# Kernel optimization log

Measured on AMD Instinct MI355X. Metric: run time of the kernel, lower is better.

The kernel has to match this reference:

```python
import jax, jax.numpy as jnp
import numpy as np

HIDDEN = 1024
VOCAB = 50257
MAX_LEN = 12


def setup_inputs() -> dict:
    key = jax.random.key(0)
    ks = jax.random.split(key, 16)
    H, V, L = HIDDEN, VOCAB, MAX_LEN
    s = 1.0 / np.sqrt(H)
    inp = {
        "input": jax.random.randint(ks[0], (1, 1), 0, V, dtype=jnp.int64),
        "h_hidden": jax.random.normal(ks[1], (1, 1, H), dtype=jnp.float32),
        "c_hidden": jax.random.normal(ks[2], (1, 1, H), dtype=jnp.float32),
        "encoder_outputs": jax.random.normal(ks[3], (L, H), dtype=jnp.float32),
        # parameters (PyTorch layout: Linear weight is [out, in])
        "emb": jax.random.normal(ks[4], (V, H), dtype=jnp.float32),
        "attn_W": jax.random.uniform(ks[5], (L, 2 * H), jnp.float32, -s, s),
        "attn_b": jax.random.uniform(ks[6], (L,), jnp.float32, -s, s),
        "comb_W": jax.random.uniform(ks[7], (H, 2 * H), jnp.float32, -s, s),
        "comb_b": jax.random.uniform(ks[8], (H,), jnp.float32, -s, s),
        "W_ih": jax.random.uniform(ks[9], (4 * H, H), jnp.float32, -s, s),
        "W_hh": jax.random.uniform(ks[10], (4 * H, H), jnp.float32, -s, s),
        "b_ih": jax.random.uniform(ks[11], (4 * H,), jnp.float32, -s, s),
        "b_hh": jax.random.uniform(ks[12], (4 * H,), jnp.float32, -s, s),
        "out_W": jax.random.uniform(ks[13], (V, H), jnp.float32, -s, s),
        "out_b": jax.random.uniform(ks[14], (V,), jnp.float32, -s, s),
    }
    return inp


def reference(input, h_hidden, c_hidden, encoder_outputs, emb, attn_W, attn_b,
              comb_W, comb_b, W_ih, W_hh, b_ih, b_hh, out_W, out_b):
    H = HIDDEN
    # embedding lookup -> [1, H] (dropout is identity in eval mode)
    embedded = emb[input.reshape(-1)].reshape(1, H)
    h0 = h_hidden[0]  # [1, H]
    c0 = c_hidden[0]  # [1, H]
    # attention weights over MAX_LEN encoder positions
    attn_in = jnp.concatenate([embedded, h0], axis=1)            # [1, 2H]
    attn_weights = jax.nn.softmax(attn_in @ attn_W.T + attn_b, axis=1)  # [1, 12]
    attn_applied = attn_weights @ encoder_outputs                # [1, H]
    # combine + relu
    x = jnp.concatenate([embedded, attn_applied], axis=1)        # [1, 2H]
    x = jax.nn.relu(x @ comb_W.T + comb_b)                       # [1, H]
    # single LSTM cell step (gate order i, f, g, o as in PyTorch)
    gates = x @ W_ih.T + b_ih + h0 @ W_hh.T + b_hh               # [1, 4H]
    i, f, g, o = jnp.split(gates, 4, axis=1)
    i, f, o = jax.nn.sigmoid(i), jax.nn.sigmoid(f), jax.nn.sigmoid(o)
    c_new = f * c0 + i * jnp.tanh(g)
    h_new = o * jnp.tanh(c_new)
    # output projection + log-softmax over vocab
    logp = jax.nn.log_softmax(h_new @ out_W.T + out_b, axis=1)   # [1, V]
    return (logp, (h_new[None], c_new[None]), attn_weights)
```

## Files before the change

### kernel.cpp

```cpp
#include <hip/hip_runtime.h>
#include <math.h>

#define HID 1024
#define VOC 50257
#define MLEN 12

__device__ __forceinline__ float wave_reduce_sum(float v) {
    for (int off = 32; off > 0; off >>= 1)
        v += __shfl_down(v, off, 64);
    return v;
}

__global__ __launch_bounds__(256) void k1_embed_attn(
    const int* __restrict__ tok_p, const float* __restrict__ h0,
    const float* __restrict__ enc, const float* __restrict__ emb,
    const float* __restrict__ attn_W, const float* __restrict__ attn_b,
    float* __restrict__ ws_xin, float* __restrict__ out_attnw)
{
    __shared__ float lds_logits[MLEN];
    __shared__ float lds_w[MLEN];
    const int t = threadIdx.x;
    const int wid = t >> 6, lane = t & 63;
    const int tok = tok_p[0];
    const float4* emb4 = (const float4*)(emb + (size_t)tok * HID);
    const float4* h04  = (const float4*)h0;
    const float4* aW4  = (const float4*)attn_W;

    for (int l = wid; l < MLEN; l += 4) {
        float s = 0.f;
        for (int k = 0; k < 8; ++k) {
            int idx = k * 64 + lane;
            float4 v = (idx < 256) ? emb4[idx] : h04[idx - 256];
            float4 w = aW4[l * 512 + idx];
            s += v.x * w.x + v.y * w.y + v.z * w.z + v.w * w.w;
        }
        s = wave_reduce_sum(s);
        if (lane == 0) lds_logits[l] = s + attn_b[l];
    }
    __syncthreads();
    if (t == 0) {
        float m = -1e30f;
        for (int l = 0; l < MLEN; ++l) m = fmaxf(m, lds_logits[l]);
        float ssum = 0.f;
        for (int l = 0; l < MLEN; ++l) { float e = expf(lds_logits[l] - m); lds_w[l] = e; ssum += e; }
        float inv = 1.f / ssum;
        for (int l = 0; l < MLEN; ++l) { lds_w[l] *= inv; out_attnw[l] = lds_w[l]; }
    }
    __syncthreads();

    const float4* enc4 = (const float4*)enc;
    float4 e = emb4[t];
    float4 acc = make_float4(0.f, 0.f, 0.f, 0.f);
    for (int l = 0; l < MLEN; ++l) {
        float wl = lds_w[l];
        float4 v = enc4[l * 256 + t];
        acc.x += wl * v.x; acc.y += wl * v.y; acc.z += wl * v.z; acc.w += wl * v.w;
    }
    float4* xin4 = (float4*)ws_xin;
    xin4[t] = e;
    xin4[256 + t] = acc;
}

__global__ __launch_bounds__(256) void k2_comb(
    const float* __restrict__ ws_xin, const float* __restrict__ comb_W,
    const float* __restrict__ comb_b, float* __restrict__ ws_x)
{
    const int wid = threadIdx.x >> 6, lane = threadIdx.x & 63;
    const int row = blockIdx.x * 4 + wid;
    const float4* W4 = (const float4*)(comb_W + (size_t)row * 2048);
    const float4* v4 = (const float4*)ws_xin;
    float s = 0.f;
    for (int k = 0; k < 8; ++k) {
        int idx = k * 64 + lane;
        float4 w = W4[idx], v = v4[idx];
        s += w.x * v.x + w.y * v.y + w.z * v.z + w.w * v.w;
    }
    s = wave_reduce_sum(s);
    if (lane == 0) ws_x[row] = fmaxf(s + comb_b[row], 0.f);
}

__global__ __launch_bounds__(256) void k3_gates(
    const float* __restrict__ ws_x, const float* __restrict__ h0,
    const float* __restrict__ W_ih, const float* __restrict__ W_hh,
    const float* __restrict__ b_ih, const float* __restrict__ b_hh,
    float* __restrict__ ws_gates)
{
    const int wid = threadIdx.x >> 6, lane = threadIdx.x & 63;
    const int row = blockIdx.x * 4 + wid;
    const float4* Wi4 = (const float4*)(W_ih + (size_t)row * HID);
    const float4* Wh4 = (const float4*)(W_hh + (size_t)row * HID);
    const float4* x4  = (const float4*)ws_x;
    const float4* h4  = (const float4*)h0;
    float s = 0.f;
    for (int k = 0; k < 4; ++k) {
        int idx = k * 64 + lane;
        float4 wi = Wi4[idx], xv = x4[idx];
        float4 wh = Wh4[idx], hv = h4[idx];
        s += wi.x * xv.x + wi.y * xv.y + wi.z * xv.z + wi.w * xv.w;
        s += wh.x * hv.x + wh.y * hv.y + wh.z * hv.z + wh.w * hv.w;
    }
    s = wave_reduce_sum(s);
    if (lane == 0) ws_gates[row] = s + b_ih[row] + b_hh[row];
}

__global__ __launch_bounds__(1024) void k4_lstm(
    const float* __restrict__ ws_gates, const float* __restrict__ c0,
    float* __restrict__ out_h, float* __restrict__ out_c, float* __restrict__ ws_h)
{
    const int t = threadIdx.x;
    float ig = ws_gates[t];
    float fg = ws_gates[HID + t];
    float gg = ws_gates[2 * HID + t];
    float og = ws_gates[3 * HID + t];
    float i = 1.f / (1.f + expf(-ig));
    float f = 1.f / (1.f + expf(-fg));
    float o = 1.f / (1.f + expf(-og));
    float g = tanhf(gg);
    float c = f * c0[t] + i * g;
    float h = o * tanhf(c);
    out_c[t] = c;
    out_h[t] = h;
    ws_h[t] = h;
}

__global__ __launch_bounds__(256) void k5_logits(
    const float* __restrict__ ws_h, const float* __restrict__ out_W,
    const float* __restrict__ out_b, float* __restrict__ out_logp)
{
    const int wid = threadIdx.x >> 6, lane = threadIdx.x & 63;
    const int row = blockIdx.x * 4 + wid;
    if (row >= VOC) return;
    const float4* W4 = (const float4*)(out_W + (size_t)row * HID);
    const float4* h4 = (const float4*)ws_h;
    float s = 0.f;
    for (int k = 0; k < 4; ++k) {
        int idx = k * 64 + lane;
        float4 w = W4[idx], h = h4[idx];
        s += w.x * h.x + w.y * h.y + w.z * h.z + w.w * h.w;
    }
    s = wave_reduce_sum(s);
    if (lane == 0) out_logp[row] = s + out_b[row];
}

__global__ __launch_bounds__(1024) void k6_lse(
    const float* __restrict__ logits, float* __restrict__ ws_lse)
{
    __shared__ float red[16];
    __shared__ float red2[16];
    const int t = threadIdx.x;
    const int wid = t >> 6, lane = t & 63;
    float m = -1e30f;
    for (int i = t; i < VOC; i += 1024) m = fmaxf(m, logits[i]);
    for (int off = 32; off > 0; off >>= 1) m = fmaxf(m, __shfl_xor(m, off, 64));
    if (lane == 0) red[wid] = m;
    __syncthreads();
    if (t == 0) {
        float mm = red[0];
        for (int w = 1; w < 16; ++w) mm = fmaxf(mm, red[w]);
        red[0] = mm;
    }
    __syncthreads();
    m = red[0];
    float s = 0.f;
    for (int i = t; i < VOC; i += 1024) s += expf(logits[i] - m);
    s = wave_reduce_sum(s);
    if (lane == 0) red2[wid] = s;
    __syncthreads();
    if (t == 0) {
        float ss = 0.f;
        for (int w = 0; w < 16; ++w) ss += red2[w];
        ws_lse[0] = m + logf(ss);
    }
}

__global__ __launch_bounds__(256) void k7_sub(
    float* __restrict__ out_logp, const float* __restrict__ ws_lse)
{
    const int i = blockIdx.x * 256 + threadIdx.x;
    if (i < VOC) out_logp[i] -= ws_lse[0];
}

extern "C" void kernel_launch(void* const* d_in, const int* in_sizes, int n_in,
                              void* d_out, int out_size, void* d_ws, size_t ws_size,
                              hipStream_t stream) {
    const int*   tok      = (const int*)d_in[0];
    const float* h_hidden = (const float*)d_in[1];
    const float* c_hidden = (const float*)d_in[2];
    const float* enc      = (const float*)d_in[3];
    const float* emb      = (const float*)d_in[4];
    const float* attn_W   = (const float*)d_in[5];
    const float* attn_b   = (const float*)d_in[6];
    const float* comb_W   = (const float*)d_in[7];
    const float* comb_b   = (const float*)d_in[8];
    const float* W_ih     = (const float*)d_in[9];
    const float* W_hh     = (const float*)d_in[10];
    const float* b_ih     = (const float*)d_in[11];
    const float* b_hh     = (const float*)d_in[12];
    const float* out_W    = (const float*)d_in[13];
    const float* out_b    = (const float*)d_in[14];

    float* out       = (float*)d_out;
    float* out_logp  = out;
    float* out_h     = out + VOC;
    float* out_c     = out + VOC + HID;
    float* out_attnw = out + VOC + 2 * HID;

    float* ws       = (float*)d_ws;
    float* ws_xin   = ws;
    float* ws_x     = ws + 2048;
    float* ws_gates = ws + 3072;
    float* ws_h     = ws + 7168;
    float* ws_lse   = ws + 8192;

    k1_embed_attn<<<1, 256, 0, stream>>>(tok, h_hidden, enc, emb, attn_W, attn_b,
                                         ws_xin, out_attnw);
    k2_comb<<<HID / 4, 256, 0, stream>>>(ws_xin, comb_W, comb_b, ws_x);
    k3_gates<<<4 * HID / 4, 256, 0, stream>>>(ws_x, h_hidden, W_ih, W_hh, b_ih, b_hh, ws_gates);
    k4_lstm<<<1, 1024, 0, stream>>>(ws_gates, c_hidden, out_h, out_c, ws_h);
    k5_logits<<<(VOC + 3) / 4, 256, 0, stream>>>(ws_h, out_W, out_b, out_logp);
    k6_lse<<<1, 1024, 0, stream>>>(out_logp, ws_lse);
    k7_sub<<<(VOC + 255) / 256, 256, 0, stream>>>(out_logp, ws_lse);
}
```

Measured before the change: 441.2 us.

## Fuse decoder step into one cooperative kernel with online log-softmax

Replaces the seven separate kernels with a single cooperative launch of 256 blocks that uses grid-wide syncs between the comb, LSTM gate, logits and normalization stages. Each block redundantly recomputes the attention softmax locally, the LSTM gates are fused with the cell update per hidden unit, and the vocab projection keeps an online max/sum so the separate log-sum-exp pass over logits is dropped. This removes launch gaps and extra global passes, but caps logits parallelism at 1024 waves and adds grid-barrier costs.

```diff
diff --git a/kernel.cpp b/kernel.cpp
--- a/kernel.cpp
+++ b/kernel.cpp
@@ -1,183 +1,221 @@
 #include <hip/hip_runtime.h>
+#include <hip/hip_cooperative_groups.h>
 #include <math.h>
+
+namespace cg = cooperative_groups;
 
 #define HID 1024
 #define VOC 50257
 #define MLEN 12
-
-__device__ __forceinline__ float wave_reduce_sum(float v) {
-    for (int off = 32; off > 0; off >>= 1)
-        v += __shfl_down(v, off, 64);
+#define NBLK 256
+#define NTHR 256
+
+__device__ __forceinline__ float wave_xor_sum(float v) {
+    for (int off = 32; off; off >>= 1) v += __shfl_xor(v, off, 64);
     return v;
 }
 
-__global__ __launch_bounds__(256) void k1_embed_attn(
+__global__ __launch_bounds__(NTHR) void fused_decoder(
     const int* __restrict__ tok_p, const float* __restrict__ h0,
-    const float* __restrict__ enc, const float* __restrict__ emb,
-    const float* __restrict__ attn_W, const float* __restrict__ attn_b,
-    float* __restrict__ ws_xin, float* __restrict__ out_attnw)
+    const float* __restrict__ c0, const float* __restrict__ enc,
+    const float* __restrict__ emb, const float* __restrict__ attn_W,
+    const float* __restrict__ attn_b, const float* __restrict__ comb_W,
+    const float* __restrict__ comb_b, const float* __restrict__ W_ih,
+    const float* __restrict__ W_hh, const float* __restrict__ b_ih,
+    const float* __restrict__ b_hh, const float* __restrict__ out_W,
+    const float* __restrict__ out_b,
+    float* __restrict__ out_logp, float* __restrict__ out_h,
+    float* __restrict__ out_c, float* __restrict__ out_attnw,
+    float* __restrict__ ws_x, float* __restrict__ ws_h,
+    float* __restrict__ ws_pm, float* __restrict__ ws_ps,
+    float* __restrict__ ws_lse)
 {
-    __shared__ float lds_logits[MLEN];
-    __shared__ float lds_w[MLEN];
-    const int t = threadIdx.x;
-    const int wid = t >> 6, lane = t & 63;
+    cg::grid_group grid = cg::this_grid();
+    __shared__ float smem[2048];
+    __shared__ float s_log[MLEN], s_w[MLEN];
+    __shared__ float rm[4], rs[4];
+    const int t = threadIdx.x, wid = t >> 6, lane = t & 63;
+    const int bid = blockIdx.x;
+    const int gw = bid * 4 + wid;
+
     const int tok = tok_p[0];
     const float4* emb4 = (const float4*)(emb + (size_t)tok * HID);
     const float4* h04  = (const float4*)h0;
-    const float4* aW4  = (const float4*)attn_W;
-
-    for (int l = wid; l < MLEN; l += 4) {
+
+    {
+        const float4* aW4 = (const float4*)attn_W;
+        for (int l = wid; l < MLEN; l += 4) {
+            float s = 0.f;
+            for (int k = 0; k < 8; ++k) {
+                int idx = k * 64 + lane;
+                float4 v = (idx < 256) ? emb4[idx] : h04[idx - 256];
+                float4 w = aW4[l * 512 + idx];
+                s += v.x * w.x + v.y * w.y + v.z * w.z + v.w * w.w;
+            }
+            s = wave_xor_sum(s);
+            if (lane == 0) s_log[l] = s + attn_b[l];
+        }
+    }
+    __syncthreads();
+    if (t == 0) {
+        float m = -1e30f;
+        for (int l = 0; l < MLEN; ++l) m = fmaxf(m, s_log[l]);
+        float ss = 0.f;
+        for (int l = 0; l < MLEN; ++l) { float e = expf(s_log[l] - m); s_w[l] = e; ss += e; }
+        float inv = 1.f / ss;
+        for (int l = 0; l < MLEN; ++l) {
+            s_w[l] *= inv;
+            if (bid == 0) out_attnw[l] = s_w[l];
+        }
+    }
+    __syncthreads();
+    {
+        const float4* enc4 = (const float4*)enc;
+        float4 e = emb4[t];
+        float4 acc = make_float4(0.f, 0.f, 0.f, 0.f);
+        for (int l = 0; l < MLEN; ++l) {
+            float wl = s_w[l];
+            float4 v = enc4[l * 256 + t];
+            acc.x += wl * v.x; acc.y += wl * v.y; acc.z += wl * v.z; acc.w += wl * v.w;
+        }
+        float4* x4 = (float4*)smem;
+        x4[t] = e;
+        x4[256 + t] = acc;
+    }
+    __syncthreads();
+
+    {
+        const int row = gw;
+        const float4* W4 = (const float4*)(comb_W + (size_t)row * 2048);
+        const float4* v4 = (const float4*)smem;
         float s = 0.f;
         for (int k = 0; k < 8; ++k) {
             int idx = k * 64 + lane;
-            float4 v = (idx < 256) ? emb4[idx] : h04[idx - 256];
-            float4 w = aW4[l * 512 + idx];
-            s += v.x * w.x + v.y * w.y + v.z * w.z + v.w * w.w;
-        }
-        s = wave_reduce_sum(s);
-        if (lane == 0) lds_logits[l] = s + attn_b[l];
-    }
-    __syncthreads();
-    if (t == 0) {
-        float m = -1e30f;
-        for (int l = 0; l < MLEN; ++l) m = fmaxf(m, lds_logits[l]);
-        float ssum = 0.f;
-        for (int l = 0; l < MLEN; ++l) { float e = expf(lds_logits[l] - m); lds_w[l] = e; ssum += e; }
-        float inv = 1.f / ssum;
-        for (int l = 0; l < MLEN; ++l) { lds_w[l] *= inv; out_attnw[l] = lds_w[l]; }
-    }
-    __syncthreads();
-
-    const float4* enc4 = (const float4*)enc;
-    float4 e = emb4[t];
-    float4 acc = make_float4(0.f, 0.f, 0.f, 0.f);
-    for (int l = 0; l < MLEN; ++l) {
-        float wl = lds_w[l];
-        float4 v = enc4[l * 256 + t];
-        acc.x += wl * v.x; acc.y += wl * v.y; acc.z += wl * v.z; acc.w += wl * v.w;
-    }
-    float4* xin4 = (float4*)ws_xin;
-    xin4[t] = e;
-    xin4[256 + t] = acc;
-}
-
-__global__ __launch_bounds__(256) void k2_comb(
-    const float* __restrict__ ws_xin, const float* __restrict__ comb_W,
-    const float* __restrict__ comb_b, float* __restrict__ ws_x)
-{
-    const int wid = threadIdx.x >> 6, lane = threadIdx.x & 63;
-    const int row = blockIdx.x * 4 + wid;
-    const float4* W4 = (const float4*)(comb_W + (size_t)row * 2048);
-    const float4* v4 = (const float4*)ws_xin;
-    float s = 0.f;
-    for (int k = 0; k < 8; ++k) {
-        int idx = k * 64 + lane;
-        float4 w = W4[idx], v = v4[idx];
-        s += w.x * v.x + w.y * v.y + w.z * v.z + w.w * v.w;
-    }
-    s = wave_reduce_sum(s);
-    if (lane == 0) ws_x[row] = fmaxf(s + comb_b[row], 0.f);
-}
-
-__global__ __launch_bounds__(256) void k3_gates(
-    const float* __restrict__ ws_x, const float* __restrict__ h0,
-    const float* __restrict__ W_ih, const float* __restrict__ W_hh,
-    const float* __restrict__ b_ih, const float* __restrict__ b_hh,
-    float* __restrict__ ws_gates)
-{
-    const int wid = threadIdx.x >> 6, lane = threadIdx.x & 63;
-    const int row = blockIdx.x * 4 + wid;
-    const float4* Wi4 = (const float4*)(W_ih + (size_t)row * HID);
-    const float4* Wh4 = (const float4*)(W_hh + (size_t)row * HID);
-    const float4* x4  = (const float4*)ws_x;
-    const float4* h4  = (const float4*)h0;
-    float s = 0.f;
-    for (int k = 0; k < 4; ++k) {
-        int idx = k * 64 + lane;
-        float4 wi = Wi4[idx], xv = x4[idx];
-        float4 wh = Wh4[idx], hv = h4[idx];
-        s += wi.x * xv.x + wi.y * xv.y + wi.z * xv.z + wi.w * xv.w;
-        s += wh.x * hv.x + wh.y * hv.y + wh.z * hv.z + wh.w * hv.w;
-    }
-    s = wave_reduce_sum(s);
-    if (lane == 0) ws_gates[row] = s + b_ih[row] + b_hh[row];
-}
-
-__global__ __launch_bounds__(1024) void k4_lstm(
-    const float* __restrict__ ws_gates, const float* __restrict__ c0,
-    float* __restrict__ out_h, float* __restrict__ out_c, float* __restrict__ ws_h)
-{
-    const int t = threadIdx.x;
-    float ig = ws_gates[t];
-    float fg = ws_gates[HID + t];
-    float gg = ws_gates[2 * HID + t];
-    float og = ws_gates[3 * HID + t];
-    float i = 1.f / (1.f + expf(-ig));
-    float f = 1.f / (1.f + expf(-fg));
-    float o = 1.f / (1.f + expf(-og));
-    float g = tanhf(gg);
-    float c = f * c0[t] + i * g;
-    float h = o * tanhf(c);
-    out_c[t] = c;
-    out_h[t] = h;
-    ws_h[t] = h;
-}
-
-__global__ __launch_bounds__(256) void k5_logits(
-    const float* __restrict__ ws_h, const float* __restrict__ out_W,
-    const float* __restrict__ out_b, float* __restrict__ out_logp)
-{
-    const int wid = threadIdx.x >> 6, lane = threadIdx.x & 63;
-    const int row = blockIdx.x * 4 + wid;
-    if (row >= VOC) return;
-    const float4* W4 = (const float4*)(out_W + (size_t)row * HID);
-    const float4* h4 = (const float4*)ws_h;
-    float s = 0.f;
-    for (int k = 0; k < 4; ++k) {
-        int idx = k * 64 + lane;
-        float4 w = W4[idx], h = h4[idx];
-        s += w.x * h.x + w.y * h.y + w.z * h.z + w.w * h.w;
-    }
-    s = wave_reduce_sum(s);
-    if (lane == 0) out_logp[row] = s + out_b[row];
-}
-
-__global__ __launch_bounds__(1024) void k6_lse(
-    const float* __restrict__ logits, float* __restrict__ ws_lse)
-{
-    __shared__ float red[16];
-    __shared__ float red2[16];
-    const int t = threadIdx.x;
-    const int wid = t >> 6, lane = t & 63;
-    float m = -1e30f;
-    for (int i = t; i < VOC; i += 1024) m = fmaxf(m, logits[i]);
-    for (int off = 32; off > 0; off >>= 1) m = fmaxf(m, __shfl_xor(m, off, 64));
-    if (lane == 0) red[wid] = m;
-    __syncthreads();
-    if (t == 0) {
-        float mm = red[0];
-        for (int w = 1; w < 16; ++w) mm = fmaxf(mm, red[w]);
-        red[0] = mm;
-    }
-    __syncthreads();
-    m = red[0];
-    float s = 0.f;
-    for (int i = t; i < VOC; i += 1024) s += expf(logits[i] - m);
-    s = wave_reduce_sum(s);
-    if (lane == 0) red2[wid] = s;
-    __syncthreads();
-    if (t == 0) {
-        float ss = 0.f;
-        for (int w = 0; w < 16; ++w) ss += red2[w];
-        ws_lse[0] = m + logf(ss);
-    }
-}
-
-__global__ __launch_bounds__(256) void k7_sub(
-    float* __restrict__ out_logp, const float* __restrict__ ws_lse)
-{
-    const int i = blockIdx.x * 256 + threadIdx.x;
-    if (i < VOC) out_logp[i] -= ws_lse[0];
+            float4 w = W4[idx], v = v4[idx];
+            s += w.x * v.x + w.y * v.y + w.z * v.z + w.w * v.w;
+        }
+        s = wave_xor_sum(s);
+        if (lane == 0) ws_x[row] = fmaxf(s + comb_b[row], 0.f);
+    }
+    __threadfence();
+    grid.sync();
+
+    {
+        float4* x4 = (float4*)smem;
+        x4[t]       = ((const float4*)ws_x)[t];
+        x4[256 + t] = h04[t];
+    }
+    __syncthreads();
+    {
+        const int h = gw;
+        float g4[4];
+        for (int g = 0; g < 4; ++g) {
+            const int row = g * HID + h;
+            const float4* Wi4 = (const float4*)(W_ih + (size_t)row * HID);
+            const float4* Wh4 = (const float4*)(W_hh + (size_t)row * HID);
+            const float4* x4  = (const float4*)smem;
+            float s = 0.f;
+            for (int k = 0; k < 4; ++k) {
+                int idx = k * 64 + lane;
+                float4 wi = Wi4[idx], xv = x4[idx];
+                float4 wh = Wh4[idx], hv = x4[256 + idx];
+                s += wi.x * xv.x + wi.y * xv.y + wi.z * xv.z + wi.w * xv.w;
+                s += wh.x * hv.x + wh.y * hv.y + wh.z * hv.z + wh.w * hv.w;
+            }
+            s = wave_xor_sum(s);
+            g4[g] = s + b_ih[row] + b_hh[row];
+        }
+        if (lane == 0) {
+            float i = 1.f / (1.f + expf(-g4[0]));
+            float f = 1.f / (1.f + expf(-g4[1]));
+            float gg = tanhf(g4[2]);
+            float o = 1.f / (1.f + expf(-g4[3]));
+            float c = f * c0[h] + i * gg;
+            float hh = o * tanhf(c);
+            out_c[h] = c;
+            out_h[h] = hh;
+            ws_h[h] = hh;
+        }
+    }
+    __threadfence();
+    grid.sync();
+
+    {
+        float4* h4w = (float4*)smem;
+        h4w[t] = ((const float4*)ws_h)[t];
+    }
+    __syncthreads();
+    {
+        const float4* h4 = (const float4*)smem;
+        float m_run = -1e30f, s_run = 0.f;
+        for (int r = gw; r < VOC; r += 2048) {
+            const int r2 = r + 1024;
+            const bool v2 = (r2 < VOC);
+            const float4* Wa = (const float4*)(out_W + (size_t)r * HID);
+            const float4* Wb = (const float4*)(out_W + (size_t)(v2 ? r2 : r) * HID);
+            float sa = 0.f, sb = 0.f;
+            for (int k = 0; k < 4; ++k) {
+                int idx = k * 64 + lane;
+                float4 hv = h4[idx];
+                float4 wa = Wa[idx];
+                sa += wa.x * hv.x + wa.y * hv.y + wa.z * hv.z + wa.w * hv.w;
+                float4 wb = Wb[idx];
+                sb += wb.x * hv.x + wb.y * hv.y + wb.z * hv.z + wb.w * hv.w;
+            }
+            sa = wave_xor_sum(sa);
+            sb = wave_xor_sum(sb);
+            sa += out_b[r];
+            if (lane == 0) out_logp[r] = sa;
+            float mn = fmaxf(m_run, sa);
+            s_run = s_run * expf(m_run - mn) + expf(sa - mn);
+            m_run = mn;
+            if (v2) {
+                sb += out_b[r2];
+                if (lane == 0) out_logp[r2] = sb;
+                mn = fmaxf(m_run, sb);
+                s_run = s_run * expf(m_run - mn) + expf(sb - mn);
+                m_run = mn;
+            }
+        }
+        if (lane == 0) { ws_pm[gw] = m_run; ws_ps[gw] = s_run; }
+    }
+    __threadfence();
+    grid.sync();
+
+    if (bid == 0) {
+        float m = -1e30f, s = 0.f;
+        for (int i = t; i < 1024; i += NTHR) {
+            float pm = ws_pm[i], ps = ws_ps[i];
+            float mn = fmaxf(m, pm);
+            s = s * expf(m - mn) + ps * expf(pm - mn);
+            m = mn;
+        }
+        for (int off = 32; off; off >>= 1) {
+            float om = __shfl_xor(m, off, 64), os = __shfl_xor(s, off, 64);
+            float mn = fmaxf(m, om);
+            s = s * expf(m - mn) + os * expf(om - mn);
+            m = mn;
+        }
+        if (lane == 0) { rm[wid] = m; rs[wid] = s; }
+        __syncthreads();
+        if (t == 0) {
+            float M = rm[0], S = rs[0];
+            for (int w = 1; w < 4; ++w) {
+                float mn = fmaxf(M, rm[w]);
+                S = S * expf(M - mn) + rs[w] * expf(rm[w] - mn);
+                M = mn;
+            }
+            ws_lse[0] = M + logf(S);
+        }
+    }
+    __threadfence();
+    grid.sync();
+
+    {
+        const float lse = ws_lse[0];
+        const int i = bid * NTHR + t;
+        if (i < VOC) out_logp[i] -= lse;
+    }
 }
 
 extern "C" void kernel_launch(void* const* d_in, const int* in_sizes, int n_in,
@@ -205,19 +243,21 @@
     float* out_c     = out + VOC + HID;
     float* out_attnw = out + VOC + 2 * HID;
 
-    float* ws       = (float*)d_ws;
-    float* ws_xin   = ws;
-    float* ws_x     = ws + 2048;
-    float* ws_gates = ws + 3072;
-    float* ws_h     = ws + 7168;
-    float* ws_lse   = ws + 8192;
-
-    k1_embed_attn<<<1, 256, 0, stream>>>(tok, h_hidden, enc, emb, attn_W, attn_b,
-                                         ws_xin, out_attnw);
-    k2_comb<<<HID / 4, 256, 0, stream>>>(ws_xin, comb_W, comb_b, ws_x);
-    k3_gates<<<4 * HID / 4, 256, 0, stream>>>(ws_x, h_hidden, W_ih, W_hh, b_ih, b_hh, ws_gates);
-    k4_lstm<<<1, 1024, 0, stream>>>(ws_gates, c_hidden, out_h, out_c, ws_h);
-    k5_logits<<<(VOC + 3) / 4, 256, 0, stream>>>(ws_h, out_W, out_b, out_logp);
-    k6_lse<<<1, 1024, 0, stream>>>(out_logp, ws_lse);
-    k7_sub<<<(VOC + 255) / 256, 256, 0, stream>>>(out_logp, ws_lse);
+    float* ws     = (float*)d_ws;
+    float* ws_x   = ws;
+    float* ws_h   = ws + 1024;
+    float* ws_pm  = ws + 2048;
+    float* ws_ps  = ws + 3072;
+    float* ws_lse = ws + 4096;
+
+    void* args[] = {
+        (void*)&tok, (void*)&h_hidden, (void*)&c_hidden, (void*)&enc,
+        (void*)&emb, (void*)&attn_W, (void*)&attn_b, (void*)&comb_W,
+        (void*)&comb_b, (void*)&W_ih, (void*)&W_hh, (void*)&b_ih,
+        (void*)&b_hh, (void*)&out_W, (void*)&out_b,
+        (void*)&out_logp, (void*)&out_h, (void*)&out_c, (void*)&out_attnw,
+        (void*)&ws_x, (void*)&ws_h, (void*)&ws_pm, (void*)&ws_ps, (void*)&ws_lse
+    };
+    hipLaunchCooperativeKernel((const void*)fused_decoder, dim3(NBLK), dim3(NTHR),
+                               args, 0, stream);
 }
```

Result: slower. 645.4 us (+46.3%).
